# Performance work log

Hardware: AMD Instinct MI355X
Metric: run time of the kernel (lower is better)

## Reference

```python
import jax, jax.numpy as jnp
import numpy as np
import math

B, N, DIM = 4, 1024, 512
H, DH = 8, 64
INNER = H * DH
K_REG, TEMP = 0.3, 0.1
LARGE_NEG = -math.log(1e10)


def setup_inputs() -> dict:
    key = jax.random.key(0)
    ks = jax.random.split(key, 10)
    x = jax.random.normal(ks[0], (B, N, DIM), dtype=jnp.float32)
    # binary float mask [b, n, n]; keep diagonal on so every row has a positive pair
    mask = (jax.random.uniform(ks[1], (B, N, N)) < 0.5).astype(jnp.float32)
    mask = jnp.maximum(mask, jnp.eye(N, dtype=jnp.float32)[None])
    s_in = 1.0 / math.sqrt(DIM)
    s_out = 1.0 / math.sqrt(INNER)
    u = lambda k, shape, s: jax.random.uniform(k, shape, jnp.float32, -s, s)
    return {
        "x": x, "attn_mask": mask,
        "Wq": u(ks[2], (INNER, DIM), s_in), "bq": u(ks[3], (INNER,), s_in),
        "Wk": u(ks[4], (INNER, DIM), s_in), "bk": u(ks[5], (INNER,), s_in),
        "Wv": u(ks[6], (INNER, DIM), s_in), "bv": u(ks[7], (INNER,), s_in),
        "Wo": u(ks[8], (DIM, INNER), s_out), "bo": u(ks[9], (DIM,), s_out),
    }


def _dynamical_contrastive_loss(scores, attn_mask, norm_matrix):
    # reconstructed from CARD's DynamicalContrastiveLoss(k, temperature)
    n = scores.shape[-1]
    cos = scores / norm_matrix / TEMP                     # [b,h,n,n]
    m = jnp.max(cos, axis=-1, keepdims=True)              # stable exp; ratio unchanged
    e = jnp.exp(cos - m)
    amask = attn_mask[:, None]                            # [b,1,n,n]
    pos = jnp.sum(e * amask, axis=-1)                     # [b,h,n]
    allsum = jnp.sum(e, axis=-1)
    clustering = -jnp.log(pos / allsum)                   # [b,h,n]
    eye = jnp.eye(n, dtype=scores.dtype)
    regular = jnp.sum(jnp.abs(eye[None] - attn_mask), axis=(-2, -1)) / (n * (n - 1))  # [b]
    loss = jnp.mean(clustering, axis=(1, 2)) + K_REG * regular
    return jnp.mean(loss)


def reference(x, attn_mask, Wq, bq, Wk, bk, Wv, bv, Wo, bo):
    b, n, _ = x.shape
    split = lambda t: t.reshape(b, n, H, DH).transpose(0, 2, 1, 3)  # b h n d
    q = split(x @ Wq.T + bq)
    k = split(x @ Wk.T + bk)
    v = split(x @ Wv.T + bv)
    scores = jnp.einsum("bhid,bhjd->bhij", q, k)
    q_norm = jnp.linalg.norm(q, axis=-1, keepdims=True)   # [b,h,n,1]
    k_norm = jnp.linalg.norm(k, axis=-1, keepdims=True)
    norm_matrix = q_norm * jnp.swapaxes(k_norm, -1, -2)   # [b,h,n,n]
    amask = attn_mask[:, None]                            # [b,1,n,n]
    masked_scores = scores * amask + jnp.where(amask == 0, LARGE_NEG, 0.0)
    dcl = _dynamical_contrastive_loss(scores, attn_mask, norm_matrix)
    scale = 1.0 / math.sqrt(DH)
    attn = jax.nn.softmax(masked_scores * scale, axis=-1)
    out = jnp.einsum("bhij,bhjd->bhid", attn, v)
    out = out.transpose(0, 2, 1, 3).reshape(b, n, INNER)
    out = out @ Wo.T + bo                                 # dropout is identity at eval
    return out, attn, dcl
```

## Files before the change

### kernel.cpp

```cpp
#include <hip/hip_runtime.h>
#include <hip/hip_bf16.h>
#include <math.h>

#define NB 4
#define NN 1024
#define DIMD 512
#define NH 8
#define DHD 64
#define INNERD 512
#define SCALE 0.125f
#define TEMPP 0.1f
#define KREG 0.3f
#define LNEG -23.025850929940457f

typedef __attribute__((ext_vector_type(8))) short bf16x8;
typedef __attribute__((ext_vector_type(4))) short bf16x4;
typedef __attribute__((ext_vector_type(4))) float f32x4;

static __device__ __forceinline__ short f2bf(float f) {
  unsigned u = __float_as_uint(f);
  u += 0x7fffu + ((u >> 16) & 1u);
  return (short)(u >> 16);
}
static __device__ __forceinline__ float bf2f(short s) {
  unsigned u = ((unsigned)(unsigned short)s) << 16;
  return __uint_as_float(u);
}

static __device__ __forceinline__ float wave_sum(float v) {
#pragma unroll
  for (int o = 1; o < 64; o <<= 1) v += __shfl_xor(v, o, 64);
  return v;
}
static __device__ __forceinline__ float wave_min(float v) {
#pragma unroll
  for (int o = 1; o < 64; o <<= 1) v = fminf(v, __shfl_xor(v, o, 64));
  return v;
}
static __device__ __forceinline__ float g16_sum(float v) {
#pragma unroll
  for (int o = 1; o < 16; o <<= 1) v += __shfl_xor(v, o, 64);
  return v;
}

__global__ __launch_bounds__(256) void k_qkv(
    const float* __restrict__ x,
    const float* __restrict__ Wq, const float* __restrict__ bq,
    const float* __restrict__ Wk, const float* __restrict__ bk,
    const float* __restrict__ Wv, const float* __restrict__ bv,
    short* __restrict__ Qb, short* __restrict__ Kb, short* __restrict__ Vb,
    float* __restrict__ qn, float* __restrict__ kn) {
  __shared__ __align__(16) short As[64][40];
  __shared__ __align__(16) short Bs[64][40];
  const int tid = threadIdx.x;
  const int lane = tid & 63;
  const int wv = tid >> 6;
  const int m0 = blockIdx.x * 64;
  const int oc = blockIdx.y;
  const int which = oc >> 3;
  const int h = oc & 7;
  const float* W = (which == 0) ? Wq : (which == 1) ? Wk : Wv;
  const float* bias = (which == 0) ? bq : (which == 1) ? bk : bv;
  short* Out = (which == 0) ? Qb : (which == 1) ? Kb : Vb;
  const int o0 = h * 64;

  const f32x4 zero4 = {0.f, 0.f, 0.f, 0.f};
  f32x4 acc[4] = {zero4, zero4, zero4, zero4};

  const int sr = tid >> 3;
  const int sc = (tid & 7) * 4;

  for (int ks = 0; ks < 16; ++ks) {
    const int k0 = ks * 32;
    __syncthreads();
#pragma unroll
    for (int t = 0; t < 2; ++t) {
      const int r = sr + t * 32;
      const f32x4 va = *reinterpret_cast<const f32x4*>(&x[(m0 + r) * DIMD + k0 + sc]);
      const f32x4 vb = *reinterpret_cast<const f32x4*>(&W[(o0 + r) * DIMD + k0 + sc]);
      bf16x4 pa, pb;
#pragma unroll
      for (int i2 = 0; i2 < 4; ++i2) { pa[i2] = f2bf(va[i2]); pb[i2] = f2bf(vb[i2]); }
      *reinterpret_cast<bf16x4*>(&As[r][sc]) = pa;
      *reinterpret_cast<bf16x4*>(&Bs[r][sc]) = pb;
    }
    __syncthreads();
    const int kk = (lane >> 4) * 8;
    const bf16x8 a = *reinterpret_cast<const bf16x8*>(&As[wv * 16 + (lane & 15)][kk]);
#pragma unroll
    for (int n = 0; n < 4; ++n) {
      const bf16x8 b = *reinterpret_cast<const bf16x8*>(&Bs[n * 16 + (lane & 15)][kk]);
      acc[n] = __builtin_amdgcn_mfma_f32_16x16x32_bf16(a, b, acc[n], 0, 0, 0);
    }
  }

  const int colb = lane & 15;
  const int rbase = m0 + wv * 16 + ((lane >> 4) << 2);
  const int bidx = m0 >> 10;
  const int hb = (bidx * NH + h) << 10;
  float p2[4] = {0.f, 0.f, 0.f, 0.f};
#pragma unroll
  for (int n = 0; n < 4; ++n) {
    const float bval = bias[o0 + n * 16 + colb];
#pragma unroll
    for (int i = 0; i < 4; ++i) {
      const float val = acc[n][i] + bval;
      p2[i] += val * val;
      const int m = rbase + i;
      Out[(long)(hb + (m & (NN - 1))) * DHD + n * 16 + colb] = f2bf(val);
    }
  }
  if (which < 2) {
    float* norm = (which == 0) ? qn : kn;
#pragma unroll
    for (int off = 1; off < 16; off <<= 1) {
#pragma unroll
      for (int i = 0; i < 4; ++i) p2[i] += __shfl_xor(p2[i], off, 64);
    }
    if (colb == 0) {
#pragma unroll
      for (int i = 0; i < 4; ++i) {
        const int m = rbase + i;
        const float nv = sqrtf(p2[i]);
        norm[hb + (m & (NN - 1))] = (which == 0) ? (1.0f / (nv * TEMPP)) : (1.0f / nv);
      }
    }
  }
}

__global__ __launch_bounds__(256) void k_vtrans(const short* __restrict__ Vb,
                                                short* __restrict__ VbT) {
  __shared__ __align__(16) short T[64][72];
  const int tid = threadIdx.x;
  const int bh = blockIdx.y;
  const int j0 = blockIdx.x * 64;
#pragma unroll
  for (int t = 0; t < 2; ++t) {
    const int idx = tid + 256 * t;
    const int r = idx >> 3, c8 = (idx & 7) * 8;
    *reinterpret_cast<bf16x8*>(&T[r][c8]) =
        *reinterpret_cast<const bf16x8*>(&Vb[(long)((bh << 10) + j0 + r) * DHD + c8]);
  }
  __syncthreads();
  const int d = tid & 63;
  const int cg = tid >> 6;
#pragma unroll
  for (int t = 0; t < 2; ++t) {
    const int ch = cg * 2 + t;
    bf16x8 v;
#pragma unroll
    for (int jj = 0; jj < 8; ++jj) v[jj] = T[ch * 8 + jj][d];
    *reinterpret_cast<bf16x8*>(&VbT[((long)(bh * DHD + d) << 10) + j0 + ch * 8]) = v;
  }
}

__global__ __launch_bounds__(256) void k_kmax(const float* __restrict__ kn,
                                              float* __restrict__ kms) {
  const int tid = threadIdx.x;
  const int bh = blockIdx.x;
  const f32x4 v = *reinterpret_cast<const f32x4*>(&kn[(bh << 10) + tid * 4]);
  float m = fminf(fminf(v[0], v[1]), fminf(v[2], v[3]));
  m = wave_min(m);
  __shared__ float red[4];
  if ((tid & 63) == 0) red[tid >> 6] = m;
  __syncthreads();
  if (tid == 0) {
    const float mn = fminf(fminf(red[0], red[1]), fminf(red[2], red[3]));
    kms[bh] = (1.0f / mn) * SCALE / TEMPP;
  }
}

static __device__ __forceinline__ short* sp(short* S, int r, int c) {
  return (short*)((char*)S + (((r << 11) + (c << 1)) ^ ((r & 7) << 4)));
}

__global__ __launch_bounds__(256) void k_attn(
    const short* __restrict__ Qb, const short* __restrict__ Kb,
    const short* __restrict__ VbT,
    const float* __restrict__ mask,
    const float* __restrict__ qn, const float* __restrict__ kn,
    const float* __restrict__ kms,
    float* __restrict__ attn, short* __restrict__ AVb,
    float* __restrict__ partial, float* __restrict__ partial2) {
  __shared__ short S[16 * 1024];
  __shared__ float rowv[16];
  __shared__ float rowscale[16];
  __shared__ float rowc[16];
  const int tid = threadIdx.x;
  const int lane = tid & 63;
  const int wv = tid >> 6;
  const int i0 = blockIdx.x * 16;
  const int bh = blockIdx.y;
  const int b = bh >> 3, h = bh & 7;

  const int lr = lane & 15;
  const int lk = lane >> 4;
  const long qoff = (long)((bh << 10) + i0 + lr) * DHD + lk * 8;
  const bf16x8 a0 = *reinterpret_cast<const bf16x8*>(&Qb[qoff]);
  const bf16x8 a1 = *reinterpret_cast<const bf16x8*>(&Qb[qoff + 32]);
  const short* Kbase = &Kb[(long)(bh << 10) * DHD];
#pragma unroll
  for (int jt = 0; jt < 16; ++jt) {
    const int j0 = wv * 256 + jt * 16;
    const long koff = (long)(j0 + lr) * DHD + lk * 8;
    const bf16x8 b0 = *reinterpret_cast<const bf16x8*>(&Kbase[koff]);
    const bf16x8 b1 = *reinterpret_cast<const bf16x8*>(&Kbase[koff + 32]);
    f32x4 acc = {0.f, 0.f, 0.f, 0.f};
    acc = __builtin_amdgcn_mfma_f32_16x16x32_bf16(a0, b0, acc, 0, 0, 0);
    acc = __builtin_amdgcn_mfma_f32_16x16x32_bf16(a1, b1, acc, 0, 0, 0);
#pragma unroll
    for (int i = 0; i < 4; ++i) *sp(S, lk * 4 + i, j0 + lr) = f2bf(acc[i]);
  }
  __syncthreads();

  const int r = tid >> 4, sub = tid & 15;
  const int gi = i0 + r;
  const float* mrow = mask + ((long)b << 20) + ((long)gi << 10);
  const float* knr = kn + (bh << 10);
  const float inv_qt = qn[(bh << 10) + gi];
  const float mlb = kms[bh] / inv_qt;
  const float argM = LNEG * SCALE - mlb;

  float Z = 0.f, alls = 0.f, pos = 0.f, cntf = 0.f;
  bf16x8 pb[8];
#pragma unroll
  for (int k = 0; k < 8; ++k) {
    const int c0 = sub * 8 + k * 128;
    const bf16x8 sv = *reinterpret_cast<const bf16x8*>(sp(S, r, c0));
    const f32x4 mv0 = *reinterpret_cast<const f32x4*>(&mrow[c0]);
    const f32x4 mv1 = *reinterpret_cast<const f32x4*>(&mrow[c0 + 4]);
    const f32x4 kn0 = *reinterpret_cast<const f32x4*>(&knr[c0]);
    const f32x4 kn1 = *reinterpret_cast<const f32x4*>(&knr[c0 + 4]);
    bf16x8 p;
#pragma unroll
    for (int e = 0; e < 8; ++e) {
      const float s = bf2f(sv[e]);
      const float mval = (e < 4) ? mv0[e] : mv1[e - 4];
      const float rk = (e < 4) ? kn0[e] : kn1[e - 4];
      const bool mset = (mval != 0.0f);
      const float a1v = mset ? (s * SCALE - mlb) : argM;
      const float ev = __expf(a1v);
      const float ec = __expf(s * inv_qt * rk - 1.0f / TEMPP);
      Z += ev;
      alls += ec;
      pos += mset ? ec : 0.0f;
      cntf += mset ? 1.0f : 0.0f;
      p[e] = f2bf(ev);
    }
    pb[k] = p;
    *reinterpret_cast<bf16x8*>(sp(S, r, c0)) = p;
  }
  Z = g16_sum(Z);
  alls = g16_sum(alls);
  pos = g16_sum(pos);
  const float rZ = 1.0f / Z;
  if (sub == 0) { rowv[r] = __logf(alls) - __logf(pos); rowscale[r] = rZ; }
  if (h == 0) {
    cntf = g16_sum(cntf);
    if (sub == 0) rowc[r] = cntf;
  }
  __syncthreads();

  float* arow = attn + ((long)bh << 20) + ((long)gi << 10);
#pragma unroll
  for (int k = 0; k < 8; ++k) {
    const int c0 = sub * 8 + k * 128;
    f32x4 o0, o1;
#pragma unroll
    for (int e = 0; e < 4; ++e) {
      o0[e] = bf2f(pb[k][e]) * rZ;
      o1[e] = bf2f(pb[k][4 + e]) * rZ;
    }
    *reinterpret_cast<f32x4*>(&arow[c0]) = o0;
    *reinterpret_cast<f32x4*>(&arow[c0 + 4]) = o1;
  }
  if (tid == 0) {
    float s = 0.f;
#pragma unroll
    for (int i = 0; i < 16; ++i) s += rowv[i];
    partial[bh * 64 + blockIdx.x] = s;
    if (h == 0) {
      float c = 0.f;
#pragma unroll
      for (int i = 0; i < 16; ++i) c += rowc[i];
      partial2[b * 64 + blockIdx.x] = c - 16.0f;
    }
  }

  f32x4 acc = {0.f, 0.f, 0.f, 0.f};
  const short* vrow = &VbT[(long)(bh * DHD + wv * 16 + lr) << 10];
#pragma unroll 8
  for (int k0 = 0; k0 < 32; ++k0) {
    const bf16x8 a = *reinterpret_cast<const bf16x8*>(sp(S, lr, k0 * 32 + lk * 8));
    const bf16x8 bb = *reinterpret_cast<const bf16x8*>(&vrow[k0 * 32 + lk * 8]);
    acc = __builtin_amdgcn_mfma_f32_16x16x32_bf16(a, bb, acc, 0, 0, 0);
  }
#pragma unroll
  for (int i = 0; i < 4; ++i) {
    const int row = lk * 4 + i;
    const float o = acc[i] * rowscale[row];
    AVb[((long)((b << 10) + i0 + row) << 9) + h * DHD + wv * 16 + lr] = f2bf(o);
  }
}

__global__ __launch_bounds__(256) void k_outproj(const short* __restrict__ AVb,
                                                 const float* __restrict__ Wo,
                                                 const float* __restrict__ bo,
                                                 float* __restrict__ out) {
  __shared__ __align__(16) short As[64][40];
  __shared__ __align__(16) short Bs[64][40];
  const int tid = threadIdx.x;
  const int lane = tid & 63, wv = tid >> 6;
  const int m0 = blockIdx.x * 64, o0 = blockIdx.y * 64;
  const f32x4 zero4 = {0.f, 0.f, 0.f, 0.f};
  f32x4 acc[4] = {zero4, zero4, zero4, zero4};
  const int ar = tid >> 2, ac = (tid & 3) * 8;
  const int br2 = tid >> 3, bc4 = (tid & 7) * 4;

  for (int ks = 0; ks < 16; ++ks) {
    const int k0 = ks * 32;
    __syncthreads();
    *reinterpret_cast<bf16x8*>(&As[ar][ac]) =
        *reinterpret_cast<const bf16x8*>(&AVb[((long)(m0 + ar) << 9) + k0 + ac]);
#pragma unroll
    for (int t = 0; t < 2; ++t) {
      const int rr = br2 + t * 32;
      const f32x4 vb = *reinterpret_cast<const f32x4*>(&Wo[(o0 + rr) * DIMD + k0 + bc4]);
      bf16x4 pbv;
#pragma unroll
      for (int i2 = 0; i2 < 4; ++i2) pbv[i2] = f2bf(vb[i2]);
      *reinterpret_cast<bf16x4*>(&Bs[rr][bc4]) = pbv;
    }
    __syncthreads();
    const int kk = (lane >> 4) * 8;
    const bf16x8 a = *reinterpret_cast<const bf16x8*>(&As[wv * 16 + (lane & 15)][kk]);
#pragma unroll
    for (int n = 0; n < 4; ++n) {
      const bf16x8 b = *reinterpret_cast<const bf16x8*>(&Bs[n * 16 + (lane & 15)][kk]);
      acc[n] = __builtin_amdgcn_mfma_f32_16x16x32_bf16(a, b, acc[n], 0, 0, 0);
    }
  }
  const int rbase = m0 + wv * 16 + ((lane >> 4) << 2);
#pragma unroll
  for (int i = 0; i < 4; ++i) {
#pragma unroll
    for (int n = 0; n < 4; ++n) {
      const int o = o0 + n * 16 + (lane & 15);
      out[((long)(rbase + i) << 9) + o] = acc[n][i] + bo[o];
    }
  }
}

__global__ __launch_bounds__(256) void k_finalize(const float* __restrict__ partial,
                                                  const float* __restrict__ partial2,
                                                  float* __restrict__ dcl) {
  const int tid = threadIdx.x;
  float s = 0.f;
#pragma unroll
  for (int t = 0; t < 8; ++t) s += partial[tid + t * 256];
  float s2 = partial2[tid];
  s = wave_sum(s);
  s2 = wave_sum(s2);
  __shared__ float red[4], red2[4];
  if ((tid & 63) == 0) { red[tid >> 6] = s; red2[tid >> 6] = s2; }
  __syncthreads();
  if (tid == 0) {
    const float cl = red[0] + red[1] + red[2] + red[3];
    const float rg = red2[0] + red2[1] + red2[2] + red2[3];
    *dcl = cl / (float)(NB * NH * NN) + KREG * rg / ((float)NN * (float)(NN - 1)) / (float)NB;
  }
}

extern "C" void kernel_launch(void* const* d_in, const int* in_sizes, int n_in,
                              void* d_out, int out_size, void* d_ws, size_t ws_size,
                              hipStream_t stream) {
  const float* x = (const float*)d_in[0];
  const float* mask = (const float*)d_in[1];
  const float* Wq = (const float*)d_in[2];
  const float* bq = (const float*)d_in[3];
  const float* Wk = (const float*)d_in[4];
  const float* bk = (const float*)d_in[5];
  const float* Wv = (const float*)d_in[6];
  const float* bv = (const float*)d_in[7];
  const float* Wo = (const float*)d_in[8];
  const float* bo = (const float*)d_in[9];

  float* out = (float*)d_out;
  float* attn = out + (size_t)NB * NN * DIMD;
  float* dcl = attn + (size_t)NB * NH * NN * NN;

  char* ws = (char*)d_ws;
  short* Qb = (short*)(ws);
  short* Kb = (short*)(ws + ((size_t)4 << 20));
  short* Vb = (short*)(ws + ((size_t)8 << 20));
  short* VbT = (short*)(ws + ((size_t)12 << 20));
  short* AVb = (short*)(ws + ((size_t)16 << 20));
  float* qn = (float*)(ws + ((size_t)20 << 20));
  float* kn = (float*)(ws + ((size_t)20 << 20) + (1 << 18));
  float* kms = (float*)(ws + ((size_t)20 << 20) + (2 << 18));
  float* partial = (float*)(ws + ((size_t)20 << 20) + (3 << 18));
  float* partial2 = (float*)(ws + ((size_t)20 << 20) + (4 << 18));

  k_qkv<<<dim3(64, 24), 256, 0, stream>>>(x, Wq, bq, Wk, bk, Wv, bv, Qb, Kb, Vb, qn, kn);
  k_vtrans<<<dim3(16, 32), 256, 0, stream>>>(Vb, VbT);
  k_kmax<<<dim3(32), 256, 0, stream>>>(kn, kms);
  k_attn<<<dim3(64, 32), 256, 0, stream>>>(Qb, Kb, VbT, mask, qn, kn, kms, attn, AVb,
                                           partial, partial2);
  k_outproj<<<dim3(64, 8), 256, 0, stream>>>(AVb, Wo, bo, out);
  k_finalize<<<1, 256, 0, stream>>>(partial, partial2, dcl);
}
```

Before: 302.4 us.

## Fuse softmax/contrastive elementwise math into QK^T MFMA epilogue in registers

Swaps the MFMA operands so each lane holds four consecutive key columns of one query row. The exp, mask and contrastive sums are then computed directly on the fp32 accumulator, and only the bf16 probabilities are written to shared memory. This drops the intermediate bf16 score round-trip through LDS and one rounding step. Row reductions now use cross-lane shuffles plus a small per-wave LDS reduction with an extra barrier, and the attn store re-reads the probabilities from LDS.

After: 303.2 us. About the same (+0.3%).

```diff
diff --git a/kernel.cpp b/kernel.cpp
--- a/kernel.cpp
+++ b/kernel.cpp
@@ -37,11 +37,6 @@
   for (int o = 1; o < 64; o <<= 1) v = fminf(v, __shfl_xor(v, o, 64));
   return v;
 }
-static __device__ __forceinline__ float g16_sum(float v) {
-#pragma unroll
-  for (int o = 1; o < 16; o <<= 1) v += __shfl_xor(v, o, 64);
-  return v;
-}
 
 __global__ __launch_bounds__(256) void k_qkv(
     const float* __restrict__ x,
@@ -183,6 +178,8 @@
     float* __restrict__ attn, short* __restrict__ AVb,
     float* __restrict__ partial, float* __restrict__ partial2) {
   __shared__ short S[16 * 1024];
+  __shared__ float red[4][16][3];
+  __shared__ float redc[4][16];
   __shared__ float rowv[16];
   __shared__ float rowscale[16];
   __shared__ float rowc[16];
@@ -195,81 +192,77 @@
 
   const int lr = lane & 15;
   const int lk = lane >> 4;
+
   const long qoff = (long)((bh << 10) + i0 + lr) * DHD + lk * 8;
-  const bf16x8 a0 = *reinterpret_cast<const bf16x8*>(&Qb[qoff]);
-  const bf16x8 a1 = *reinterpret_cast<const bf16x8*>(&Qb[qoff + 32]);
+  const bf16x8 q0 = *reinterpret_cast<const bf16x8*>(&Qb[qoff]);
+  const bf16x8 q1 = *reinterpret_cast<const bf16x8*>(&Qb[qoff + 32]);
   const short* Kbase = &Kb[(long)(bh << 10) * DHD];
+  const float* mrow = mask + ((long)b << 20) + ((long)(i0 + lr) << 10);
+  const float* knr = kn + (bh << 10);
+  const float inv_qt = qn[(bh << 10) + i0 + lr];
+  const float mlb = kms[bh] / inv_qt;
+  const float argM = LNEG * SCALE - mlb;
+
+  float Z = 0.f, alls = 0.f, pos = 0.f, cntf = 0.f;
 #pragma unroll
   for (int jt = 0; jt < 16; ++jt) {
     const int j0 = wv * 256 + jt * 16;
     const long koff = (long)(j0 + lr) * DHD + lk * 8;
-    const bf16x8 b0 = *reinterpret_cast<const bf16x8*>(&Kbase[koff]);
-    const bf16x8 b1 = *reinterpret_cast<const bf16x8*>(&Kbase[koff + 32]);
+    const bf16x8 k0 = *reinterpret_cast<const bf16x8*>(&Kbase[koff]);
+    const bf16x8 k1 = *reinterpret_cast<const bf16x8*>(&Kbase[koff + 32]);
     f32x4 acc = {0.f, 0.f, 0.f, 0.f};
-    acc = __builtin_amdgcn_mfma_f32_16x16x32_bf16(a0, b0, acc, 0, 0, 0);
-    acc = __builtin_amdgcn_mfma_f32_16x16x32_bf16(a1, b1, acc, 0, 0, 0);
-#pragma unroll
-    for (int i = 0; i < 4; ++i) *sp(S, lk * 4 + i, j0 + lr) = f2bf(acc[i]);
-  }
-  __syncthreads();
-
-  const int r = tid >> 4, sub = tid & 15;
-  const int gi = i0 + r;
-  const float* mrow = mask + ((long)b << 20) + ((long)gi << 10);
-  const float* knr = kn + (bh << 10);
-  const float inv_qt = qn[(bh << 10) + gi];
-  const float mlb = kms[bh] / inv_qt;
-  const float argM = LNEG * SCALE - mlb;
-
-  float Z = 0.f, alls = 0.f, pos = 0.f, cntf = 0.f;
-  bf16x8 pb[8];
-#pragma unroll
-  for (int k = 0; k < 8; ++k) {
-    const int c0 = sub * 8 + k * 128;
-    const bf16x8 sv = *reinterpret_cast<const bf16x8*>(sp(S, r, c0));
-    const f32x4 mv0 = *reinterpret_cast<const f32x4*>(&mrow[c0]);
-    const f32x4 mv1 = *reinterpret_cast<const f32x4*>(&mrow[c0 + 4]);
-    const f32x4 kn0 = *reinterpret_cast<const f32x4*>(&knr[c0]);
-    const f32x4 kn1 = *reinterpret_cast<const f32x4*>(&knr[c0 + 4]);
-    bf16x8 p;
-#pragma unroll
-    for (int e = 0; e < 8; ++e) {
-      const float s = bf2f(sv[e]);
-      const float mval = (e < 4) ? mv0[e] : mv1[e - 4];
-      const float rk = (e < 4) ? kn0[e] : kn1[e - 4];
-      const bool mset = (mval != 0.0f);
-      const float a1v = mset ? (s * SCALE - mlb) : argM;
-      const float ev = __expf(a1v);
-      const float ec = __expf(s * inv_qt * rk - 1.0f / TEMPP);
+    acc = __builtin_amdgcn_mfma_f32_16x16x32_bf16(k0, q0, acc, 0, 0, 0);
+    acc = __builtin_amdgcn_mfma_f32_16x16x32_bf16(k1, q1, acc, 0, 0, 0);
+    const int jl = j0 + lk * 4;
+    const f32x4 mv = *reinterpret_cast<const f32x4*>(&mrow[jl]);
+    const f32x4 kv = *reinterpret_cast<const f32x4*>(&knr[jl]);
+    bf16x4 p;
+#pragma unroll
+    for (int e = 0; e < 4; ++e) {
+      const float s = acc[e];
+      const bool mset = (mv[e] != 0.0f);
+      const float ev = __expf(mset ? (s * SCALE - mlb) : argM);
+      const float ec = __expf(__builtin_fmaf(s * inv_qt, kv[e], -1.0f / TEMPP));
       Z += ev;
       alls += ec;
       pos += mset ? ec : 0.0f;
       cntf += mset ? 1.0f : 0.0f;
       p[e] = f2bf(ev);
     }
-    pb[k] = p;
-    *reinterpret_cast<bf16x8*>(sp(S, r, c0)) = p;
-  }
-  Z = g16_sum(Z);
-  alls = g16_sum(alls);
-  pos = g16_sum(pos);
-  const float rZ = 1.0f / Z;
-  if (sub == 0) { rowv[r] = __logf(alls) - __logf(pos); rowscale[r] = rZ; }
+    *reinterpret_cast<bf16x4*>(sp(S, lr, jl)) = p;
+  }
+  Z += __shfl_xor(Z, 16, 64);    Z += __shfl_xor(Z, 32, 64);
+  alls += __shfl_xor(alls, 16, 64); alls += __shfl_xor(alls, 32, 64);
+  pos += __shfl_xor(pos, 16, 64);  pos += __shfl_xor(pos, 32, 64);
+  if (lk == 0) { red[wv][lr][0] = Z; red[wv][lr][1] = alls; red[wv][lr][2] = pos; }
   if (h == 0) {
-    cntf = g16_sum(cntf);
-    if (sub == 0) rowc[r] = cntf;
+    cntf += __shfl_xor(cntf, 16, 64); cntf += __shfl_xor(cntf, 32, 64);
+    if (lk == 0) redc[wv][lr] = cntf;
   }
   __syncthreads();
 
-  float* arow = attn + ((long)bh << 20) + ((long)gi << 10);
+  const int r = tid >> 4, sub = tid & 15;
+  if (sub == 0) {
+    const float Zt = red[0][r][0] + red[1][r][0] + red[2][r][0] + red[3][r][0];
+    const float at = red[0][r][1] + red[1][r][1] + red[2][r][1] + red[3][r][1];
+    const float pt = red[0][r][2] + red[1][r][2] + red[2][r][2] + red[3][r][2];
+    rowscale[r] = 1.0f / Zt;
+    rowv[r] = __logf(at) - __logf(pt);
+    if (h == 0) rowc[r] = redc[0][r] + redc[1][r] + redc[2][r] + redc[3][r];
+  }
+  __syncthreads();
+
+  const float rZ = rowscale[r];
+  float* arow = attn + ((long)bh << 20) + ((long)(i0 + r) << 10);
 #pragma unroll
   for (int k = 0; k < 8; ++k) {
     const int c0 = sub * 8 + k * 128;
+    const bf16x8 sv = *reinterpret_cast<const bf16x8*>(sp(S, r, c0));
     f32x4 o0, o1;
 #pragma unroll
     for (int e = 0; e < 4; ++e) {
-      o0[e] = bf2f(pb[k][e]) * rZ;
-      o1[e] = bf2f(pb[k][4 + e]) * rZ;
+      o0[e] = bf2f(sv[e]) * rZ;
+      o1[e] = bf2f(sv[4 + e]) * rZ;
     }
     *reinterpret_cast<f32x4*>(&arow[c0]) = o0;
     *reinterpret_cast<f32x4*>(&arow[c0 + 4]) = o1;
@@ -287,18 +280,18 @@
     }
   }
 
-  f32x4 acc = {0.f, 0.f, 0.f, 0.f};
+  f32x4 acc2 = {0.f, 0.f, 0.f, 0.f};
   const short* vrow = &VbT[(long)(bh * DHD + wv * 16 + lr) << 10];
 #pragma unroll 8
   for (int k0 = 0; k0 < 32; ++k0) {
     const bf16x8 a = *reinterpret_cast<const bf16x8*>(sp(S, lr, k0 * 32 + lk * 8));
     const bf16x8 bb = *reinterpret_cast<const bf16x8*>(&vrow[k0 * 32 + lk * 8]);
-    acc = __builtin_amdgcn_mfma_f32_16x16x32_bf16(a, bb, acc, 0, 0, 0);
+    acc2 = __builtin_amdgcn_mfma_f32_16x16x32_bf16(a, bb, acc2, 0, 0, 0);
   }
 #pragma unroll
   for (int i = 0; i < 4; ++i) {
     const int row = lk * 4 + i;
-    const float o = acc[i] * rowscale[row];
+    const float o = acc2[i] * rowscale[row];
     AVb[((long)((b << 10) + i0 + row) << 9) + h * DHD + wv * 16 + lr] = f2bf(o);
   }
 }
```
